# Kernel optimization log

Hardware: AMD Instinct MI355X
Metric: run time of the kernel (lower is better)

## Reference

```python
import jax, jax.numpy as jnp
import numpy as np

N_NODES = 100000
N_EDGES = 1600000
DIM = 64
N_GRAPHS = 1000


def setup_inputs() -> dict:
    key = jax.random.key(0)
    ks = jax.random.split(key, 6)
    s = 1.0 / np.sqrt(DIM)
    x = jax.random.normal(ks[0], (N_NODES, DIM), dtype=jnp.float32)
    edge_index = jax.random.randint(ks[1], (2, N_EDGES), 0, N_NODES, dtype=jnp.int64)
    batch = jnp.sort(jax.random.randint(ks[2], (N_NODES,), 0, N_GRAPHS, dtype=jnp.int64))
    W1 = jax.random.normal(ks[3], (DIM, DIM), dtype=jnp.float32) * s
    b1 = jnp.zeros((DIM,), jnp.float32)
    W2 = jax.random.normal(ks[4], (DIM, DIM), dtype=jnp.float32) * s
    b2 = jnp.zeros((DIM,), jnp.float32)
    return {"x": x, "W1": W1, "b1": b1, "W2": W2, "b2": b2,
            "edge_index": edge_index, "batch": batch}


def reference(x, W1, b1, W2, b2, edge_index, batch):
    n = x.shape[0]
    loop = jnp.arange(n, dtype=edge_index.dtype)
    src = jnp.concatenate([edge_index[0], loop])  # [E+N] with self-loops
    dst = jnp.concatenate([edge_index[1], loop])
    # symmetric GCN normalization: deg^{-1/2}[src] * deg^{-1/2}[dst]
    deg = jax.ops.segment_sum(jnp.ones(src.shape[0], x.dtype), dst, num_segments=n)
    dinv = jax.lax.rsqrt(jnp.maximum(deg, 1.0))  # deg >= 1 due to self-loops
    norm = (dinv[src] * dinv[dst])[:, None]      # [E+N, 1]

    def gcn(h, W, b):
        h = h @ W                                  # transform first (smaller dim path)
        msg = h[src] * norm                        # gather + normalize
        return jax.ops.segment_sum(msg, dst, num_segments=n) + b

    h = jax.nn.relu(gcn(x, W1, b1))
    # dropout: eval mode -> identity
    h = jax.nn.relu(gcn(h, W2, b2))

    counts = jax.ops.segment_sum(jnp.ones((n,), x.dtype), batch, num_segments=N_GRAPHS)
    pooled = jax.ops.segment_sum(h, batch, num_segments=N_GRAPHS)
    return pooled / jnp.maximum(counts, 1.0)[:, None]
```

## Files before the change

kernel.cpp:

```cpp
#include <hip/hip_runtime.h>
#include <hip/hip_fp16.h>

#define DIM 64
#define BIN_SHIFT 7
#define BINSZ 128
#define MAXBINS 1024
#define PB 512
#define PB_LOG 9

typedef __attribute__((ext_vector_type(2))) float floatx2;
typedef __attribute__((ext_vector_type(4))) float f32x4;
typedef __attribute__((ext_vector_type(8))) _Float16 f16x8;
typedef __attribute__((ext_vector_type(4))) _Float16 f16x4;


__global__ __launch_bounds__(256) void k_hist(const int* __restrict__ dst,
                                              int* __restrict__ C, int E, int NB) {
    __shared__ int h[MAXBINS];
    for (int i = threadIdx.x; i < NB; i += 256) h[i] = 0;
    __syncthreads();
    int per = (E + PB - 1) / PB;
    int e0 = blockIdx.x * per;
    int e1 = e0 + per; if (e1 > E) e1 = E;
    for (int e = e0 + (int)threadIdx.x; e < e1; e += 256)
        atomicAdd(&h[dst[e] >> BIN_SHIFT], 1);
    __syncthreads();
    for (int i = threadIdx.x; i < NB; i += 256)
        C[blockIdx.x * NB + i] = h[i];
}


__global__ __launch_bounds__(1024) void k_scanA(const int* __restrict__ C,
                                                int* __restrict__ S,
                                                int* __restrict__ bsums, int NB, int M) {
    __shared__ int sh[1024];
    int tid = threadIdx.x;
    int j0 = blockIdx.x * 4096 + tid * 4;
    int v[4]; int sum = 0;
#pragma unroll
    for (int t = 0; t < 4; ++t) {
        int j = j0 + t; int x = 0;
        if (j < M) { int bin = j >> PB_LOG, blk = j & (PB - 1); x = C[blk * NB + bin]; }
        v[t] = sum; sum += x;
    }
    sh[tid] = sum;
    __syncthreads();
#pragma unroll
    for (int d = 1; d < 1024; d <<= 1) {
        int t = (tid >= d) ? sh[tid - d] : 0;
        __syncthreads();
        sh[tid] += t;
        __syncthreads();
    }
    int excl = sh[tid] - sum;
#pragma unroll
    for (int t = 0; t < 4; ++t) {
        int j = j0 + t;
        if (j < M) S[j] = excl + v[t];
    }
    if (tid == 1023) bsums[blockIdx.x] = sh[1023];
}


__global__ __launch_bounds__(1024) void k_scanB(int* __restrict__ bsums, int nb) {
    __shared__ int s[1024];
    int tid = threadIdx.x;
    int v = (tid < nb) ? bsums[tid] : 0;
    s[tid] = v;
    __syncthreads();
#pragma unroll
    for (int d = 1; d < 1024; d <<= 1) {
        int t = (tid >= d) ? s[tid - d] : 0;
        __syncthreads();
        s[tid] += t;
        __syncthreads();
    }
    if (tid < nb) bsums[tid] = s[tid] - v;
}


__global__ __launch_bounds__(256) void k_bucket(const int* __restrict__ src,
                                                const int* __restrict__ dst,
                                                const int* __restrict__ S,
                                                const int* __restrict__ bsums,
                                                int* __restrict__ bkt, int E, int NB) {
    __shared__ int lcur[MAXBINS];
    int blk = blockIdx.x;
    for (int i = threadIdx.x; i < NB; i += 256) {
        int j = i * PB + blk;
        lcur[i] = S[j] + bsums[j >> 12];
    }
    __syncthreads();
    int per = (E + PB - 1) / PB;
    int e0 = blk * per;
    int e1 = e0 + per; if (e1 > E) e1 = E;
    for (int e = e0 + (int)threadIdx.x; e < e1; e += 256) {
        int d = dst[e];
        int pos = atomicAdd(&lcur[d >> BIN_SHIFT], 1);
        bkt[pos] = src[e] | ((d & (BINSZ - 1)) << 24);
    }
}


__global__ __launch_bounds__(256) void k_binsort(const int* __restrict__ bkt,
                                                 const int* __restrict__ S,
                                                 const int* __restrict__ bsums,
                                                 int* __restrict__ csr,
                                                 int* __restrict__ off,
                                                 float* __restrict__ dinv,
                                                 const int* __restrict__ batch,
                                                 int* __restrict__ goff,
                                                 int N, int G, int E, int NB) {
    __shared__ int cnt[BINSZ], bas[BINSZ], cur[BINSZ];
    __shared__ int wsum[4];
    int tid = threadIdx.x;
    int b = blockIdx.x;
    int j0 = b << PB_LOG;
    int s0 = S[j0] + bsums[j0 >> 12];
    int s1 = E;
    if (b + 1 < NB) { int j1 = (b + 1) << PB_LOG; s1 = S[j1] + bsums[j1 >> 12]; }
    if (tid < BINSZ) { cnt[tid] = 0; cur[tid] = 0; }
    __syncthreads();
    for (int i = s0 + tid; i < s1; i += 256)
        atomicAdd(&cnt[(bkt[i] >> 24) & (BINSZ - 1)], 1);
    __syncthreads();
    int my = (tid < BINSZ) ? cnt[tid] : 0;
    int lane = tid & 63, wv = tid >> 6;
    int x = my;
#pragma unroll
    for (int d = 1; d < 64; d <<= 1) {
        int t = __shfl_up(x, d);
        if (lane >= d) x += t;
    }
    if (lane == 63) wsum[wv] = x;
    __syncthreads();
    int prefix = 0;
    for (int w = 0; w < wv; ++w) prefix += wsum[w];
    int ex = x + prefix - my;
    if (tid < BINSZ) {
        bas[tid] = ex;
        int v = (b << BIN_SHIFT) + tid;
        if (v < N) {
            off[v] = s0 + ex;
            dinv[v] = rsqrtf((float)(my + 1));
            if (v == N - 1) off[N] = E;
            int bb = batch[v];
            int prev = (v == 0) ? -1 : batch[v - 1];
            for (int g = prev + 1; g <= bb; ++g) goff[g] = v;
            if (v == N - 1)
                for (int g = bb + 1; g <= G; ++g) goff[g] = N;
        }
    }
    __syncthreads();
    for (int i = s0 + tid; i < s1; i += 256) {
        int p = bkt[i];
        int lo = (p >> 24) & (BINSZ - 1);
        int li = atomicAdd(&cur[lo], 1);
        csr[s0 + bas[lo] + li] = p & 0xFFFFFF;
    }
}


__global__ __launch_bounds__(256) void k_gemm(const float* __restrict__ X,
                                              const float* __restrict__ W,
                                              const float* __restrict__ dinv,
                                              unsigned int* __restrict__ Y8, int N) {
    __shared__ float Os[16 * 68];
    int tid = threadIdx.x;
    int lane = tid & 63, w = tid >> 6;
    int m = lane & 15, g = lane >> 4;
    int row0 = blockIdx.x * 16;
    int row = row0 + m;

    f16x8 B0, B1;
    {
        int n = (w << 4) + m;
        const float* wp = W + (g << 3) * 64 + n;
#pragma unroll
        for (int j = 0; j < 8; ++j) B0[j] = (_Float16)wp[j * 64];
        wp += 32 * 64;
#pragma unroll
        for (int j = 0; j < 8; ++j) B1[j] = (_Float16)wp[j * 64];
    }
    f16x8 A0, A1;
    {
        float4 u0 = make_float4(0.f, 0.f, 0.f, 0.f), u1 = u0, u2 = u0, u3 = u0;
        if (row < N) {
            const float* xp = X + (size_t)row * DIM + (g << 3);
            u0 = *(const float4*)(xp);
            u1 = *(const float4*)(xp + 4);
            u2 = *(const float4*)(xp + 32);
            u3 = *(const float4*)(xp + 36);
        }
        A0[0] = (_Float16)u0.x; A0[1] = (_Float16)u0.y; A0[2] = (_Float16)u0.z; A0[3] = (_Float16)u0.w;
        A0[4] = (_Float16)u1.x; A0[5] = (_Float16)u1.y; A0[6] = (_Float16)u1.z; A0[7] = (_Float16)u1.w;
        A1[0] = (_Float16)u2.x; A1[1] = (_Float16)u2.y; A1[2] = (_Float16)u2.z; A1[3] = (_Float16)u2.w;
        A1[4] = (_Float16)u3.x; A1[5] = (_Float16)u3.y; A1[6] = (_Float16)u3.z; A1[7] = (_Float16)u3.w;
    }
    f32x4 acc = {0.f, 0.f, 0.f, 0.f};
    acc = __builtin_amdgcn_mfma_f32_16x16x32_f16(A0, B0, acc, 0, 0, 0);
    acc = __builtin_amdgcn_mfma_f32_16x16x32_f16(A1, B1, acc, 0, 0, 0);
#pragma unroll
    for (int j = 0; j < 4; ++j)
        Os[((g << 2) + j) * 68 + (w << 4) + m] = acc[j];
    __syncthreads();

    int r = tid >> 4, c = tid & 15;
    int orow = row0 + r;
    if (orow < N) {
        float4 o = *(const float4*)(Os + r * 68 + (c << 2));
        float s = dinv[orow];
        int p = 0;
        p = __builtin_amdgcn_cvt_pk_fp8_f32(o.x * s, o.y * s, p, false);
        p = __builtin_amdgcn_cvt_pk_fp8_f32(o.z * s, o.w * s, p, true);
        Y8[(size_t)orow * 16 + c] = (unsigned int)p;
    } else if (orow == N) {
        Y8[(size_t)orow * 16 + c] = 0u;
    }
}


__device__ __forceinline__ float4 gather_rows(const unsigned int* __restrict__ hs8,
                                              const int* __restrict__ csr,
                                              int k0, int k1, int v, int l, int gw4,
                                              int N) {
    float4 a0, a1, a2, a3;
    {
        unsigned int u = hs8[(unsigned)((v << 4) | l)];
        floatx2 f0 = __builtin_amdgcn_cvt_pk_f32_fp8((int)u, false);
        floatx2 f1 = __builtin_amdgcn_cvt_pk_f32_fp8((int)u, true);
        a0 = make_float4(f0.x, f0.y, f1.x, f1.y);
        a1 = make_float4(0.f, 0.f, 0.f, 0.f);
        a2 = make_float4(0.f, 0.f, 0.f, 0.f);
        a3 = make_float4(0.f, 0.f, 0.f, 0.f);
    }
    for (int kb = k0; kb < k1; kb += 16) {
        int rem = k1 - kb;
        int idx = (l < rem) ? csr[kb + l] : N;
        int mm = rem < 16 ? rem : 16;
        for (int j = 0; j < mm; j += 8) {
            int s0 = __shfl(idx, gw4 + j + 0);
            int s1 = __shfl(idx, gw4 + j + 1);
            int s2 = __shfl(idx, gw4 + j + 2);
            int s3 = __shfl(idx, gw4 + j + 3);
            int s4 = __shfl(idx, gw4 + j + 4);
            int s5 = __shfl(idx, gw4 + j + 5);
            int s6 = __shfl(idx, gw4 + j + 6);
            int s7 = __shfl(idx, gw4 + j + 7);
            unsigned int u0 = hs8[(unsigned)((s0 << 4) | l)];
            unsigned int u1 = hs8[(unsigned)((s1 << 4) | l)];
            unsigned int u2 = hs8[(unsigned)((s2 << 4) | l)];
            unsigned int u3 = hs8[(unsigned)((s3 << 4) | l)];
            unsigned int u4 = hs8[(unsigned)((s4 << 4) | l)];
            unsigned int u5 = hs8[(unsigned)((s5 << 4) | l)];
            unsigned int u6 = hs8[(unsigned)((s6 << 4) | l)];
            unsigned int u7 = hs8[(unsigned)((s7 << 4) | l)];
            floatx2 p0l = __builtin_amdgcn_cvt_pk_f32_fp8((int)u0, false);
            floatx2 p0h = __builtin_amdgcn_cvt_pk_f32_fp8((int)u0, true);
            floatx2 p1l = __builtin_amdgcn_cvt_pk_f32_fp8((int)u1, false);
            floatx2 p1h = __builtin_amdgcn_cvt_pk_f32_fp8((int)u1, true);
            floatx2 p2l = __builtin_amdgcn_cvt_pk_f32_fp8((int)u2, false);
            floatx2 p2h = __builtin_amdgcn_cvt_pk_f32_fp8((int)u2, true);
            floatx2 p3l = __builtin_amdgcn_cvt_pk_f32_fp8((int)u3, false);
            floatx2 p3h = __builtin_amdgcn_cvt_pk_f32_fp8((int)u3, true);
            floatx2 p4l = __builtin_amdgcn_cvt_pk_f32_fp8((int)u4, false);
            floatx2 p4h = __builtin_amdgcn_cvt_pk_f32_fp8((int)u4, true);
            floatx2 p5l = __builtin_amdgcn_cvt_pk_f32_fp8((int)u5, false);
            floatx2 p5h = __builtin_amdgcn_cvt_pk_f32_fp8((int)u5, true);
            floatx2 p6l = __builtin_amdgcn_cvt_pk_f32_fp8((int)u6, false);
            floatx2 p6h = __builtin_amdgcn_cvt_pk_f32_fp8((int)u6, true);
            floatx2 p7l = __builtin_amdgcn_cvt_pk_f32_fp8((int)u7, false);
            floatx2 p7h = __builtin_amdgcn_cvt_pk_f32_fp8((int)u7, true);
            a0.x += p0l.x; a0.y += p0l.y; a0.z += p0h.x; a0.w += p0h.y;
            a1.x += p1l.x; a1.y += p1l.y; a1.z += p1h.x; a1.w += p1h.y;
            a2.x += p2l.x; a2.y += p2l.y; a2.z += p2h.x; a2.w += p2h.y;
            a3.x += p3l.x; a3.y += p3l.y; a3.z += p3h.x; a3.w += p3h.y;
            a0.x += p4l.x; a0.y += p4l.y; a0.z += p4h.x; a0.w += p4h.y;
            a1.x += p5l.x; a1.y += p5l.y; a1.z += p5h.x; a1.w += p5h.y;
            a2.x += p6l.x; a2.y += p6l.y; a2.z += p6h.x; a2.w += p6h.y;
            a3.x += p7l.x; a3.y += p7l.y; a3.z += p7h.x; a3.w += p7h.y;
        }
    }
    return make_float4(a0.x + a1.x + a2.x + a3.x,
                       a0.y + a1.y + a2.y + a3.y,
                       a0.z + a1.z + a2.z + a3.z,
                       a0.w + a1.w + a2.w + a3.w);
}


__global__ __launch_bounds__(256) void k_gather_gemm(const unsigned int* __restrict__ hs8,
                                                     const int* __restrict__ csr,
                                                     const int* __restrict__ off,
                                                     const float* __restrict__ dinv,
                                                     const float* __restrict__ bias,
                                                     const float* __restrict__ W,
                                                     unsigned int* __restrict__ hs_out,
                                                     int N) {
    __shared__ _Float16 Xs[16 * 72];
    __shared__ float Os[16 * 68];
    int tid = threadIdx.x;
    int r = tid >> 4, l = tid & 15;
    int lane = tid & 63, w = tid >> 6;
    int m = lane & 15, g = lane >> 4;
    int gw4 = (r & 3) << 4;
    int v = blockIdx.x * 16 + r;

    f16x8 B0, B1;
    {
        int n = (w << 4) + m;
        const float* wp = W + (g << 3) * 64 + n;
#pragma unroll
        for (int j = 0; j < 8; ++j) B0[j] = (_Float16)wp[j * 64];
        wp += 32 * 64;
#pragma unroll
        for (int j = 0; j < 8; ++j) B1[j] = (_Float16)wp[j * 64];
    }
    if (blockIdx.x == 0 && tid < 16)
        hs_out[(size_t)N * 16 + tid] = 0u;

    float dv = 0.f;
    float4 h = make_float4(0.f, 0.f, 0.f, 0.f);
    if (v < N) {
        dv = dinv[v];
        float4 bv = ((const float4*)bias)[l];
        float4 acc = gather_rows(hs8, csr, off[v], off[v + 1], v, l, gw4, N);
        h.x = fmaxf(acc.x * dv + bv.x, 0.f);
        h.y = fmaxf(acc.y * dv + bv.y, 0.f);
        h.z = fmaxf(acc.z * dv + bv.z, 0.f);
        h.w = fmaxf(acc.w * dv + bv.w, 0.f);
    }
    {
        f16x4 hv;
        hv[0] = (_Float16)h.x; hv[1] = (_Float16)h.y;
        hv[2] = (_Float16)h.z; hv[3] = (_Float16)h.w;
        *(f16x4*)(Xs + r * 72 + (l << 2)) = hv;
    }
    __syncthreads();

    f16x8 A0 = *(const f16x8*)(Xs + m * 72 + (g << 3));
    f16x8 A1 = *(const f16x8*)(Xs + m * 72 + 32 + (g << 3));
    f32x4 acc2 = {0.f, 0.f, 0.f, 0.f};
    acc2 = __builtin_amdgcn_mfma_f32_16x16x32_f16(A0, B0, acc2, 0, 0, 0);
    acc2 = __builtin_amdgcn_mfma_f32_16x16x32_f16(A1, B1, acc2, 0, 0, 0);
#pragma unroll
    for (int j = 0; j < 4; ++j)
        Os[((g << 2) + j) * 68 + (w << 4) + m] = acc2[j];
    __syncthreads();

    if (v < N) {
        float4 o = *(const float4*)(Os + r * 68 + (l << 2));
        int p = 0;
        p = __builtin_amdgcn_cvt_pk_fp8_f32(o.x * dv, o.y * dv, p, false);
        p = __builtin_amdgcn_cvt_pk_fp8_f32(o.z * dv, o.w * dv, p, true);
        hs_out[(size_t)v * 16 + l] = (unsigned int)p;
    }
}


__global__ __launch_bounds__(256) void k_gather16(const unsigned int* __restrict__ hs8,
                                                  const int* __restrict__ csr,
                                                  const int* __restrict__ off,
                                                  const float* __restrict__ dinv,
                                                  const float* __restrict__ bias,
                                                  __half* __restrict__ agg, int N) {
    int tid = threadIdx.x;
    int v = blockIdx.x * 16 + (tid >> 4);
    if (v >= N) return;
    int l = tid & 15;
    int gw4 = ((tid >> 4) & 3) << 4;
    float dv = dinv[v];
    float4 bv = ((const float4*)bias)[l];
    float4 acc = gather_rows(hs8, csr, off[v], off[v + 1], v, l, gw4, N);
    __half2 p0 = __floats2half2_rn(acc.x * dv + bv.x, acc.y * dv + bv.y);
    __half2 p1 = __floats2half2_rn(acc.z * dv + bv.z, acc.w * dv + bv.w);
    uint2 u;
    u.x = *(unsigned int*)&p0;
    u.y = *(unsigned int*)&p1;
    ((uint2*)(agg + (size_t)v * DIM))[l] = u;
}


__global__ __launch_bounds__(256) void k_pool(const __half* __restrict__ agg,
                                              const int* __restrict__ goff,
                                              float* __restrict__ out, int G) {
    int g = blockIdx.x * 4 + (threadIdx.x >> 6);
    if (g >= G) return;
    int lane = threadIdx.x & 63;
    int q = lane >> 4, c = lane & 15;
    const uint2* h2 = (const uint2*)agg;
    int n0 = goff[g], n1 = goff[g + 1];
    float4 acc = make_float4(0.f, 0.f, 0.f, 0.f);
    for (int i = n0 + q; i < n1; i += 4) {
        uint2 u = h2[(size_t)i * 16 + c];
        float2 f0 = __half22float2(*(__half2*)&u.x);
        float2 f1 = __half22float2(*(__half2*)&u.y);
        acc.x += fmaxf(f0.x, 0.f); acc.y += fmaxf(f0.y, 0.f);
        acc.z += fmaxf(f1.x, 0.f); acc.w += fmaxf(f1.y, 0.f);
    }
    acc.x += __shfl_down(acc.x, 32); acc.y += __shfl_down(acc.y, 32);
    acc.z += __shfl_down(acc.z, 32); acc.w += __shfl_down(acc.w, 32);
    acc.x += __shfl_down(acc.x, 16); acc.y += __shfl_down(acc.y, 16);
    acc.z += __shfl_down(acc.z, 16); acc.w += __shfl_down(acc.w, 16);
    if (q == 0) {
        float inv = 1.0f / fmaxf((float)(n1 - n0), 1.0f);
        *(float4*)(out + ((size_t)g << 6) + (c << 2)) =
            make_float4(acc.x * inv, acc.y * inv, acc.z * inv, acc.w * inv);
    }
}


static inline int cdiv(int a, int b) { return (a + b - 1) / b; }

extern "C" void kernel_launch(void* const* d_in, const int* in_sizes, int n_in,
                              void* d_out, int out_size, void* d_ws, size_t ws_size,
                              hipStream_t stream) {
    const float* x   = (const float*)d_in[0];
    const float* W1  = (const float*)d_in[1];
    const float* b1  = (const float*)d_in[2];
    const float* W2  = (const float*)d_in[3];
    const float* b2  = (const float*)d_in[4];
    const int*   ei  = (const int*)d_in[5];
    const int*   bat = (const int*)d_in[6];

    const int N = in_sizes[0] / DIM;
    const int E = in_sizes[5] / 2;
    const int G = out_size / DIM;
    const int NB = cdiv(N, BINSZ);
    const int M  = NB * PB;
    const int* src = ei;
    const int* dst = ei + E;
    float* out = (float*)d_out;

    __half* hs1    = (__half*)d_ws;
    __half* hs2    = hs1 + (size_t)(N + 1) * DIM;
    __half* agg1   = hs2 + (size_t)(N + 1) * DIM;
    float*  dinv   = (float*)(agg1 + (size_t)N * DIM);
    int*    off    = (int*)(dinv + N);
    int*    goff   = off + (N + 1);
    int*    C      = goff + (G + 1);
    int*    S      = C + (size_t)PB * NB;
    int*    bsums  = S + (size_t)PB * NB;
    int*    csr    = bsums + 1024;
    int*    bkt    = (int*)hs1;
    __half* agg2   = hs1;

    k_hist<<<PB, 256, 0, stream>>>(dst, C, E, NB);
    int nb2 = cdiv(M, 4096);
    k_scanA<<<nb2, 1024, 0, stream>>>(C, S, bsums, NB, M);
    k_scanB<<<1, 1024, 0, stream>>>(bsums, nb2);
    k_bucket<<<PB, 256, 0, stream>>>(src, dst, S, bsums, bkt, E, NB);
    k_binsort<<<NB, 256, 0, stream>>>(bkt, S, bsums, csr, off, dinv, bat, goff, N, G, E, NB);

    k_gemm<<<cdiv(N + 1, 16), 256, 0, stream>>>(x, W1, dinv, (unsigned int*)hs1, N);

    k_gather_gemm<<<cdiv(N, 16), 256, 0, stream>>>((const unsigned int*)hs1, csr, off,
                                                   dinv, b1, W2, (unsigned int*)hs2, N);

    k_gather16<<<cdiv(N, 16), 256, 0, stream>>>((const unsigned int*)hs2, csr, off,
                                                dinv, b2, agg2, N);

    k_pool<<<cdiv(G, 4), 256, 0, stream>>>(agg2, goff, out, G);
}
```

Before: 203.6 us.

## Fuse final gather with mean pooling via atomics and batch gather loads

The second-layer gather kernel now applies ReLU, scales each node's row by 1/graph size, and adds it straight into the output with atomics. Rows in a block that belong to the same graph are first summed in shared memory, so the fp16 aggregate buffer and the separate pool kernel are no longer needed. The output is zeroed inside the binsort kernel. The gather loop is also rewritten to issue all 16 neighbour loads before converting them, which raises memory-level parallelism. In exchange it adds float atomics, whose summation order is nondeterministic, and it issues loads for padded index slots that point to the dummy row.

```diff
diff --git a/kernel.cpp b/kernel.cpp
--- a/kernel.cpp
+++ b/kernel.cpp
@@ -110,11 +110,13 @@
                                                  float* __restrict__ dinv,
                                                  const int* __restrict__ batch,
                                                  int* __restrict__ goff,
+                                                 float* __restrict__ outz,
                                                  int N, int G, int E, int NB) {
     __shared__ int cnt[BINSZ], bas[BINSZ], cur[BINSZ];
     __shared__ int wsum[4];
     int tid = threadIdx.x;
     int b = blockIdx.x;
+    for (int i = b * 256 + tid; i < G * DIM; i += NB * 256) outz[i] = 0.f;
     int j0 = b << PB_LOG;
     int s0 = S[j0] + bsums[j0 >> 12];
     int s1 = E;
@@ -237,48 +239,26 @@
     for (int kb = k0; kb < k1; kb += 16) {
         int rem = k1 - kb;
         int idx = (l < rem) ? csr[kb + l] : N;
-        int mm = rem < 16 ? rem : 16;
-        for (int j = 0; j < mm; j += 8) {
-            int s0 = __shfl(idx, gw4 + j + 0);
-            int s1 = __shfl(idx, gw4 + j + 1);
-            int s2 = __shfl(idx, gw4 + j + 2);
-            int s3 = __shfl(idx, gw4 + j + 3);
-            int s4 = __shfl(idx, gw4 + j + 4);
-            int s5 = __shfl(idx, gw4 + j + 5);
-            int s6 = __shfl(idx, gw4 + j + 6);
-            int s7 = __shfl(idx, gw4 + j + 7);
-            unsigned int u0 = hs8[(unsigned)((s0 << 4) | l)];
-            unsigned int u1 = hs8[(unsigned)((s1 << 4) | l)];
-            unsigned int u2 = hs8[(unsigned)((s2 << 4) | l)];
-            unsigned int u3 = hs8[(unsigned)((s3 << 4) | l)];
-            unsigned int u4 = hs8[(unsigned)((s4 << 4) | l)];
-            unsigned int u5 = hs8[(unsigned)((s5 << 4) | l)];
-            unsigned int u6 = hs8[(unsigned)((s6 << 4) | l)];
-            unsigned int u7 = hs8[(unsigned)((s7 << 4) | l)];
-            floatx2 p0l = __builtin_amdgcn_cvt_pk_f32_fp8((int)u0, false);
-            floatx2 p0h = __builtin_amdgcn_cvt_pk_f32_fp8((int)u0, true);
-            floatx2 p1l = __builtin_amdgcn_cvt_pk_f32_fp8((int)u1, false);
-            floatx2 p1h = __builtin_amdgcn_cvt_pk_f32_fp8((int)u1, true);
-            floatx2 p2l = __builtin_amdgcn_cvt_pk_f32_fp8((int)u2, false);
-            floatx2 p2h = __builtin_amdgcn_cvt_pk_f32_fp8((int)u2, true);
-            floatx2 p3l = __builtin_amdgcn_cvt_pk_f32_fp8((int)u3, false);
-            floatx2 p3h = __builtin_amdgcn_cvt_pk_f32_fp8((int)u3, true);
-            floatx2 p4l = __builtin_amdgcn_cvt_pk_f32_fp8((int)u4, false);
-            floatx2 p4h = __builtin_amdgcn_cvt_pk_f32_fp8((int)u4, true);
-            floatx2 p5l = __builtin_amdgcn_cvt_pk_f32_fp8((int)u5, false);
-            floatx2 p5h = __builtin_amdgcn_cvt_pk_f32_fp8((int)u5, true);
-            floatx2 p6l = __builtin_amdgcn_cvt_pk_f32_fp8((int)u6, false);
-            floatx2 p6h = __builtin_amdgcn_cvt_pk_f32_fp8((int)u6, true);
-            floatx2 p7l = __builtin_amdgcn_cvt_pk_f32_fp8((int)u7, false);
-            floatx2 p7h = __builtin_amdgcn_cvt_pk_f32_fp8((int)u7, true);
-            a0.x += p0l.x; a0.y += p0l.y; a0.z += p0h.x; a0.w += p0h.y;
-            a1.x += p1l.x; a1.y += p1l.y; a1.z += p1h.x; a1.w += p1h.y;
-            a2.x += p2l.x; a2.y += p2l.y; a2.z += p2h.x; a2.w += p2h.y;
-            a3.x += p3l.x; a3.y += p3l.y; a3.z += p3h.x; a3.w += p3h.y;
-            a0.x += p4l.x; a0.y += p4l.y; a0.z += p4h.x; a0.w += p4h.y;
-            a1.x += p5l.x; a1.y += p5l.y; a1.z += p5h.x; a1.w += p5h.y;
-            a2.x += p6l.x; a2.y += p6l.y; a2.z += p6h.x; a2.w += p6h.y;
-            a3.x += p7l.x; a3.y += p7l.y; a3.z += p7h.x; a3.w += p7h.y;
+        unsigned uu[16];
+#pragma unroll
+        for (int t = 0; t < 16; ++t) {
+            int s = __shfl(idx, gw4 + t);
+            uu[t] = hs8[(unsigned)((s << 4) | l)];
+        }
+#pragma unroll
+        for (int t = 0; t < 16; t += 4) {
+            floatx2 q0 = __builtin_amdgcn_cvt_pk_f32_fp8((int)uu[t + 0], false);
+            floatx2 q1 = __builtin_amdgcn_cvt_pk_f32_fp8((int)uu[t + 0], true);
+            floatx2 q2 = __builtin_amdgcn_cvt_pk_f32_fp8((int)uu[t + 1], false);
+            floatx2 q3 = __builtin_amdgcn_cvt_pk_f32_fp8((int)uu[t + 1], true);
+            floatx2 q4 = __builtin_amdgcn_cvt_pk_f32_fp8((int)uu[t + 2], false);
+            floatx2 q5 = __builtin_amdgcn_cvt_pk_f32_fp8((int)uu[t + 2], true);
+            floatx2 q6 = __builtin_amdgcn_cvt_pk_f32_fp8((int)uu[t + 3], false);
+            floatx2 q7 = __builtin_amdgcn_cvt_pk_f32_fp8((int)uu[t + 3], true);
+            a0.x += q0.x; a0.y += q0.y; a0.z += q1.x; a0.w += q1.y;
+            a1.x += q2.x; a1.y += q2.y; a1.z += q3.x; a1.w += q3.y;
+            a2.x += q4.x; a2.y += q4.y; a2.z += q5.x; a2.w += q5.y;
+            a3.x += q6.x; a3.y += q6.y; a3.z += q7.x; a3.w += q7.y;
         }
     }
     return make_float4(a0.x + a1.x + a2.x + a3.x,
@@ -357,54 +337,52 @@
 }
 
 
-__global__ __launch_bounds__(256) void k_gather16(const unsigned int* __restrict__ hs8,
-                                                  const int* __restrict__ csr,
-                                                  const int* __restrict__ off,
-                                                  const float* __restrict__ dinv,
-                                                  const float* __restrict__ bias,
-                                                  __half* __restrict__ agg, int N) {
-    int tid = threadIdx.x;
-    int v = blockIdx.x * 16 + (tid >> 4);
-    if (v >= N) return;
-    int l = tid & 15;
-    int gw4 = ((tid >> 4) & 3) << 4;
-    float dv = dinv[v];
-    float4 bv = ((const float4*)bias)[l];
-    float4 acc = gather_rows(hs8, csr, off[v], off[v + 1], v, l, gw4, N);
-    __half2 p0 = __floats2half2_rn(acc.x * dv + bv.x, acc.y * dv + bv.y);
-    __half2 p1 = __floats2half2_rn(acc.z * dv + bv.z, acc.w * dv + bv.w);
-    uint2 u;
-    u.x = *(unsigned int*)&p0;
-    u.y = *(unsigned int*)&p1;
-    ((uint2*)(agg + (size_t)v * DIM))[l] = u;
-}
-
-
-__global__ __launch_bounds__(256) void k_pool(const __half* __restrict__ agg,
-                                              const int* __restrict__ goff,
-                                              float* __restrict__ out, int G) {
-    int g = blockIdx.x * 4 + (threadIdx.x >> 6);
-    if (g >= G) return;
-    int lane = threadIdx.x & 63;
-    int q = lane >> 4, c = lane & 15;
-    const uint2* h2 = (const uint2*)agg;
-    int n0 = goff[g], n1 = goff[g + 1];
-    float4 acc = make_float4(0.f, 0.f, 0.f, 0.f);
-    for (int i = n0 + q; i < n1; i += 4) {
-        uint2 u = h2[(size_t)i * 16 + c];
-        float2 f0 = __half22float2(*(__half2*)&u.x);
-        float2 f1 = __half22float2(*(__half2*)&u.y);
-        acc.x += fmaxf(f0.x, 0.f); acc.y += fmaxf(f0.y, 0.f);
-        acc.z += fmaxf(f1.x, 0.f); acc.w += fmaxf(f1.y, 0.f);
-    }
-    acc.x += __shfl_down(acc.x, 32); acc.y += __shfl_down(acc.y, 32);
-    acc.z += __shfl_down(acc.z, 32); acc.w += __shfl_down(acc.w, 32);
-    acc.x += __shfl_down(acc.x, 16); acc.y += __shfl_down(acc.y, 16);
-    acc.z += __shfl_down(acc.z, 16); acc.w += __shfl_down(acc.w, 16);
-    if (q == 0) {
-        float inv = 1.0f / fmaxf((float)(n1 - n0), 1.0f);
-        *(float4*)(out + ((size_t)g << 6) + (c << 2)) =
-            make_float4(acc.x * inv, acc.y * inv, acc.z * inv, acc.w * inv);
+__global__ __launch_bounds__(256) void k_gather_pool(const unsigned int* __restrict__ hs8,
+                                                     const int* __restrict__ csr,
+                                                     const int* __restrict__ off,
+                                                     const float* __restrict__ dinv,
+                                                     const float* __restrict__ bias,
+                                                     const int* __restrict__ batch,
+                                                     const int* __restrict__ goff,
+                                                     float* __restrict__ out, int N) {
+    __shared__ float vals[16][68];
+    __shared__ int gid[16];
+    int tid = threadIdx.x;
+    int r = tid >> 4, l = tid & 15;
+    int gw4 = (r & 3) << 4;
+    int v = blockIdx.x * 16 + r;
+
+    float4 val = make_float4(0.f, 0.f, 0.f, 0.f);
+    int g = -1;
+    if (v < N) {
+        g = batch[v];
+        float dv = dinv[v];
+        float4 bv = ((const float4*)bias)[l];
+        float4 acc = gather_rows(hs8, csr, off[v], off[v + 1], v, l, gw4, N);
+        float inv = 1.0f / (float)(goff[g + 1] - goff[g]);
+        val.x = fmaxf(acc.x * dv + bv.x, 0.f) * inv;
+        val.y = fmaxf(acc.y * dv + bv.y, 0.f) * inv;
+        val.z = fmaxf(acc.z * dv + bv.z, 0.f) * inv;
+        val.w = fmaxf(acc.w * dv + bv.w, 0.f) * inv;
+    }
+    *(float4*)(&vals[r][l << 2]) = val;
+    if (l == 0) gid[r] = g;
+    __syncthreads();
+
+    if (v < N) {
+        bool leader = (r == 0) || (gid[r - 1] != g);
+        if (leader) {
+            float4 s = val;
+            for (int rr = r + 1; rr < 16 && gid[rr] == g; ++rr) {
+                float4 t = *(const float4*)(&vals[rr][l << 2]);
+                s.x += t.x; s.y += t.y; s.z += t.z; s.w += t.w;
+            }
+            float* op = out + (size_t)g * DIM + (l << 2);
+            atomicAdd(op + 0, s.x);
+            atomicAdd(op + 1, s.y);
+            atomicAdd(op + 2, s.z);
+            atomicAdd(op + 3, s.w);
+        }
     }
 }
 
@@ -433,8 +411,8 @@
 
     __half* hs1    = (__half*)d_ws;
     __half* hs2    = hs1 + (size_t)(N + 1) * DIM;
-    __half* agg1   = hs2 + (size_t)(N + 1) * DIM;
-    float*  dinv   = (float*)(agg1 + (size_t)N * DIM);
+    __half* spare  = hs2 + (size_t)(N + 1) * DIM;
+    float*  dinv   = (float*)(spare + (size_t)N * DIM);
     int*    off    = (int*)(dinv + N);
     int*    goff   = off + (N + 1);
     int*    C      = goff + (G + 1);
@@ -442,22 +420,20 @@
     int*    bsums  = S + (size_t)PB * NB;
     int*    csr    = bsums + 1024;
     int*    bkt    = (int*)hs1;
-    __half* agg2   = hs1;
 
     k_hist<<<PB, 256, 0, stream>>>(dst, C, E, NB);
     int nb2 = cdiv(M, 4096);
     k_scanA<<<nb2, 1024, 0, stream>>>(C, S, bsums, NB, M);
     k_scanB<<<1, 1024, 0, stream>>>(bsums, nb2);
     k_bucket<<<PB, 256, 0, stream>>>(src, dst, S, bsums, bkt, E, NB);
-    k_binsort<<<NB, 256, 0, stream>>>(bkt, S, bsums, csr, off, dinv, bat, goff, N, G, E, NB);
+    k_binsort<<<NB, 256, 0, stream>>>(bkt, S, bsums, csr, off, dinv, bat, goff,
+                                      out, N, G, E, NB);
 
     k_gemm<<<cdiv(N + 1, 16), 256, 0, stream>>>(x, W1, dinv, (unsigned int*)hs1, N);
 
     k_gather_gemm<<<cdiv(N, 16), 256, 0, stream>>>((const unsigned int*)hs1, csr, off,
                                                    dinv, b1, W2, (unsigned int*)hs2, N);
 
-    k_gather16<<<cdiv(N, 16), 256, 0, stream>>>((const unsigned int*)hs2, csr, off,
-                                                dinv, b2, agg2, N);
-
-    k_pool<<<cdiv(G, 4), 256, 0, stream>>>(agg2, goff, out, G);
-}
+    k_gather_pool<<<cdiv(N, 16), 256, 0, stream>>>((const unsigned int*)hs2, csr, off,
+                                                   dinv, b2, bat, goff, out, N);
+}
```

Result: faster. 197.2 us (-3.1%).
